# Kernel optimization log

Hardware: AMD Instinct MI355X
Metric: run time of the kernel (lower is better)

Reference implementation:

```python
import jax, jax.numpy as jnp
import numpy as np

D_MODEL, D_QKV, N_HEADS = 1024, 64, 16


def setup_inputs() -> dict:
    key = jax.random.key(0)
    k_x, k_qkv, k_out = jax.random.split(key, 3)
    X = jax.random.normal(k_x, (2, 2048, D_MODEL), dtype=jnp.float32)
    # nn.Linear(d_model, 3*d_qkv*n_heads, bias=False): store as (in, out) for X @ W
    W_qkv = jax.random.normal(k_qkv, (D_MODEL, 3 * D_QKV * N_HEADS), dtype=jnp.float32) * (D_MODEL ** -0.5)
    W_out = jax.random.normal(k_out, (D_QKV * N_HEADS, D_MODEL), dtype=jnp.float32) * ((D_QKV * N_HEADS) ** -0.5)
    return {"X": X, "W_qkv": W_qkv, "W_out": W_out}


def reference(X, W_qkv, W_out):
    b, s, _ = X.shape
    h, d = N_HEADS, D_QKV
    scale = d ** 0.5
    qkv = X @ W_qkv                          # [b, s, 3*h*d]
    # Faithful to torch: view(b, s, h, d, 3).unbind(-1) -> interleaved q/k/v layout
    qkv = qkv.reshape(b, s, h, d, 3)
    q, k, v = qkv[..., 0], qkv[..., 1], qkv[..., 2]   # each [b, s, h, d]
    scores = jnp.einsum("bqhd,bkhd->bhqk", q, k) / scale
    weights = jax.nn.softmax(scores, axis=-1)          # [b, h, s, s]
    attn = jnp.einsum("bhqk,bkhd->bqhd", weights, v)   # [b, s, h, d]
    return attn.reshape(b, s, h * d) @ W_out           # [b, s, d_model]
```

## Files before the change

kernel.cpp:

```cpp
#include <hip/hip_runtime.h>
#include <hip/hip_bf16.h>
#include <math.h>

typedef __bf16 bf16;
typedef __bf16 bf16x2 __attribute__((ext_vector_type(2)));
typedef __bf16 bf16x4 __attribute__((ext_vector_type(4)));
typedef __bf16 bf16x8 __attribute__((ext_vector_type(8)));
typedef float f32x4 __attribute__((ext_vector_type(4)));
typedef float f32x16 __attribute__((ext_vector_type(16)));
typedef int i32x2 __attribute__((ext_vector_type(2)));
typedef int i32x4 __attribute__((ext_vector_type(4)));

#define MFMA16(a, b, c) __builtin_amdgcn_mfma_f32_16x16x32_bf16(a, b, c, 0, 0, 0)
#define MFMA32(a, b, c) __builtin_amdgcn_mfma_f32_32x32x16_bf16(a, b, c, 0, 0, 0)

constexpr int D_MODEL = 1024;
constexpr int N_QKV   = 3072;
constexpr int BATCH   = 2;
constexpr int SEQ     = 2048;
constexpr int NH      = 16;
constexpr int DH      = 64;
constexpr int M_TOT   = BATCH * SEQ;

__device__ __forceinline__ void gl_lds16(const bf16* g, bf16* l) {
    __builtin_amdgcn_global_load_lds(
        (const __attribute__((address_space(1))) void*)g,
        (__attribute__((address_space(3))) void*)l, 16, 0, 0);
}

__device__ __forceinline__ void pl32swap(int& a, int& b) {
    i32x2 r = __builtin_amdgcn_permlane32_swap(a, b, false, false);
    a = r[0];
    b = r[1];
}

__device__ __forceinline__ void transpose_tile(
    const float* __restrict__ in, bf16* __restrict__ out,
    int K, int N, int n0, int k0, bf16 (*T)[72], bool permute)
{
    const int tid = threadIdx.x;
    const int r   = tid >> 2;
    const int c4  = (tid & 3) * 16;

    const float* src = in + (size_t)(k0 + r) * N + n0 + c4;
    f32x4 v0 = *(const f32x4*)(src + 0);
    f32x4 v1 = *(const f32x4*)(src + 4);
    f32x4 v2 = *(const f32x4*)(src + 8);
    f32x4 v3 = *(const f32x4*)(src + 12);
    #pragma unroll
    for (int j = 0; j < 4; j++) {
        T[c4 + j][r]      = (bf16)v0[j];
        T[c4 + 4 + j][r]  = (bf16)v1[j];
        T[c4 + 8 + j][r]  = (bf16)v2[j];
        T[c4 + 12 + j][r] = (bf16)v3[j];
    }
    __syncthreads();
    int rowg = n0 + r;
    if (permute) {
        const int which = rowg % 3;
        const int h     = rowg / 192;
        const int d     = (rowg % 192) / 3;
        rowg = which * 1024 + h * 64 + d;
    }
    bf16* dst = out + (size_t)rowg * K + k0 + c4;
    *(bf16x8*)(dst)     = *(const bf16x8*)&T[r][c4];
    *(bf16x8*)(dst + 8) = *(const bf16x8*)&T[r][c4 + 8];
}

__global__ __launch_bounds__(256) void prepass_kernel(
    const float* __restrict__ X, const float* __restrict__ Wqkv,
    const float* __restrict__ Wout,
    bf16* __restrict__ xb, bf16* __restrict__ wqkv_t, bf16* __restrict__ wout_t)
{
    __shared__ bf16 T[64][72];
    const int b = blockIdx.x;
    if (b < 2048) {
        const size_t i = ((size_t)b * 256 + threadIdx.x) * 8;
        f32x4 a0 = *(const f32x4*)(X + i);
        f32x4 a1 = *(const f32x4*)(X + i + 4);
        bf16x8 w;
        #pragma unroll
        for (int j = 0; j < 4; j++) { w[j] = (bf16)a0[j]; w[j + 4] = (bf16)a1[j]; }
        *(bf16x8*)(xb + i) = w;
    } else if (b < 2048 + 768) {
        const int idx = b - 2048;
        transpose_tile(Wqkv, wqkv_t, D_MODEL, N_QKV,
                       (idx % 48) * 64, (idx / 48) * 64, T, true);
    } else {
        const int idx = b - 2816;
        transpose_tile(Wout, wout_t, D_MODEL, D_MODEL,
                       (idx % 16) * 64, (idx / 16) * 64, T, false);
    }
}

__global__ __launch_bounds__(256) void qkv_gemm_kernel(
    const bf16* __restrict__ Xb, const bf16* __restrict__ Wt,
    bf16* __restrict__ qb, bf16* __restrict__ kb, bf16* __restrict__ vb)
{
    __shared__ __align__(16) bf16 smem[2 * 128 * 64];
    bf16* As = smem;
    bf16* Bs = smem + 128 * 64;

    const int tid  = threadIdx.x;
    const int wave = tid >> 6;
    const int lane = tid & 63;
    const int quad = lane >> 4;
    const int l16  = lane & 15;
    const int sw   = l16 & 7;
    const int m0   = blockIdx.x * 128;
    const int n0   = blockIdx.y * 128;
    const int wm   = (wave & 1) * 64;
    const int wn   = (wave >> 1) * 64;

    const int srow = lane >> 3;
    const int sc_s = ((lane & 7) ^ srow) * 8;
    const int sc_d = (lane & 7) * 8;

    f32x4 acc[4][4];
    #pragma unroll
    for (int a = 0; a < 4; a++)
        #pragma unroll
        for (int b = 0; b < 4; b++) acc[a][b] = {0.f, 0.f, 0.f, 0.f};

    for (int kb0 = 0; kb0 < D_MODEL; kb0 += 64) {
        __syncthreads();
        #pragma unroll
        for (int j = 0; j < 4; j++) {
            const int row = wave * 32 + j * 8 + srow;
            gl_lds16(Xb + (size_t)(m0 + row) * D_MODEL + kb0 + sc_s,
                     As + row * 64 + sc_d);
            gl_lds16(Wt + (size_t)(n0 + row) * D_MODEL + kb0 + sc_s,
                     Bs + row * 64 + sc_d);
        }
        __syncthreads();

        #pragma unroll
        for (int ks = 0; ks < 2; ks++) {
            const int co = ((ks * 4 + quad) ^ sw) * 8;
            bf16x8 af[4], bfr[4];
            #pragma unroll
            for (int mi = 0; mi < 4; mi++)
                af[mi] = *(const bf16x8*)&As[(wm + mi * 16 + l16) * 64 + co];
            #pragma unroll
            for (int ni = 0; ni < 4; ni++)
                bfr[ni] = *(const bf16x8*)&Bs[(wn + ni * 16 + l16) * 64 + co];
            #pragma unroll
            for (int mi = 0; mi < 4; mi++)
                #pragma unroll
                for (int ni = 0; ni < 4; ni++)
                    acc[mi][ni] = MFMA16(af[mi], bfr[ni], acc[mi][ni]);
        }
    }

    const int bb = m0 >> 11;
    if (n0 < 2048) {
        bf16* dst0 = (n0 < 1024) ? qb : kb;
        #pragma unroll
        for (int ni = 0; ni < 4; ni++) {
            const int n = n0 + wn + ni * 16 + l16;
            const int h = (n >> 6) & 15;
            const int d = n & 63;
            #pragma unroll
            for (int mi = 0; mi < 4; mi++) {
                const int s0 = (m0 + wm + mi * 16 + quad * 4) & (SEQ - 1);
                const size_t bh = (size_t)(bb * NH + h);
                #pragma unroll
                for (int i = 0; i < 4; i++)
                    dst0[(bh * SEQ + s0 + i) * DH + d] = (bf16)acc[mi][ni][i];
            }
        }
    } else {
        __syncthreads();
        bf16* T = smem;
        #pragma unroll
        for (int ni = 0; ni < 4; ni++) {
            const int nl = wn + ni * 16 + l16;
            #pragma unroll
            for (int mi = 0; mi < 4; mi++) {
                const int ml = wm + mi * 16 + quad * 4;
                bf16x4 pv;
                #pragma unroll
                for (int i = 0; i < 4; i++) pv[i] = (bf16)acc[mi][ni][i];
                const int c   = ml >> 3;
                const int swz = (c & 8) | ((c ^ nl) & 7);
                *(bf16x4*)&T[nl * 128 + swz * 8 + (ml & 7)] = pv;
            }
        }
        __syncthreads();
        const int hbase  = (n0 - 2048) >> 6;
        const int s_base = m0 & (SEQ - 1);
        #pragma unroll
        for (int it = 0; it < 8; it++) {
            const int nl = (tid >> 4) + it * 16;
            const int mc = tid & 15;
            const int swz = (mc & 8) | ((mc ^ nl) & 7);
            bf16x8 vv = *(const bf16x8*)&T[nl * 128 + swz * 8];
            const int h = hbase + (nl >> 6);
            const int d = nl & 63;
            *(bf16x8*)(vb + ((size_t)(bb * NH + h) * DH + d) * SEQ
                       + s_base + mc * 8) = vv;
        }
    }
}

__global__ __launch_bounds__(256) void attn_kernel(
    const bf16* __restrict__ qb, const bf16* __restrict__ kb,
    const bf16* __restrict__ vb, bf16* __restrict__ ob)
{
    __shared__ __align__(16) bf16 Ks[2][64 * 64];
    __shared__ __align__(16) bf16 Vt[2][64 * 64];

    const int tid  = threadIdx.x;
    const int wave = tid >> 6;
    const int lane = tid & 63;
    const int l32  = lane & 31;
    const int hi   = lane >> 5;
    const int bh   = blockIdx.x;
    const int q0   = blockIdx.y * 128;
    const size_t base = (size_t)bh * SEQ * DH;

    constexpr float QSCALE = 0.125f * 1.44269504f;

    bf16x8 qf[4];
    {
        const size_t qoff = base + (size_t)(q0 + wave * 32 + l32) * DH + hi * 8;
        #pragma unroll
        for (int kc = 0; kc < 4; kc++) {
            qf[kc] = *(const bf16x8*)(qb + qoff + kc * 16);
            #pragma unroll
            for (int j = 0; j < 8; j++)
                qf[kc][j] = (bf16)((float)qf[kc][j] * QSCALE);
        }
    }

    bf16x8 ones;
    #pragma unroll
    for (int j = 0; j < 8; j++) ones[j] = (bf16)1.0f;

    f32x16 o_acc[2];
    f32x16 o_l;
    #pragma unroll
    for (int i = 0; i < 16; i++) {
        o_acc[0][i] = 0.f; o_acc[1][i] = 0.f; o_l[i] = 0.f;
    }

    const int so0 = tid;
    const int so1 = 256 + tid;
    const int sr0 = so0 >> 3, sc0 = ((so0 & 7) ^ (sr0 & 7)) * 8;
    const int sr1 = so1 >> 3, sc1 = ((so1 & 7) ^ (sr1 & 7)) * 8;

    #define STAGE(bufi, kk0)                                                   \
        do {                                                                   \
            gl_lds16(kb + base + (size_t)((kk0) + sr0) * DH + sc0,             \
                     &Ks[bufi][so0 * 8]);                                      \
            gl_lds16(kb + base + (size_t)((kk0) + sr1) * DH + sc1,             \
                     &Ks[bufi][so1 * 8]);                                      \
            gl_lds16(vb + base + (size_t)sr0 * SEQ + (kk0) + sc0,              \
                     &Vt[bufi][so0 * 8]);                                      \
            gl_lds16(vb + base + (size_t)sr1 * SEQ + (kk0) + sc1,              \
                     &Vt[bufi][so1 * 8]);                                      \
        } while (0)

    STAGE(0, 0);
    int buf = 0;

    for (int k0 = 0; k0 < SEQ; k0 += 64) {
        __syncthreads();
        if (k0 + 64 < SEQ) STAGE(buf ^ 1, k0 + 64);

        f32x16 sacc[2];
        #pragma unroll
        for (int i = 0; i < 16; i++) { sacc[0][i] = 0.f; sacc[1][i] = 0.f; }
        #pragma unroll
        for (int kc = 0; kc < 4; kc++) {
            #pragma unroll
            for (int kblk = 0; kblk < 2; kblk++) {
                const int key = kblk * 32 + l32;
                bf16x8 kf = *(const bf16x8*)
                    &Ks[buf][key * 64 + ((2 * kc + hi) ^ (l32 & 7)) * 8];
                sacc[kblk] = MFMA32(kf, qf[kc], sacc[kblk]);
            }
        }

        bf16x8 pa[4];
        #pragma unroll
        for (int kblk = 0; kblk < 2; kblk++) {
            int w[8];
            #pragma unroll
            for (int c = 0; c < 8; c++) {
                bf16x2 t;
                t[0] = (bf16)__builtin_amdgcn_exp2f(sacc[kblk][2 * c]);
                t[1] = (bf16)__builtin_amdgcn_exp2f(sacc[kblk][2 * c + 1]);
                w[c] = __builtin_bit_cast(int, t);
            }
            #pragma unroll
            for (int cc = 0; cc < 2; cc++) {
                pl32swap(w[cc * 4 + 0], w[cc * 4 + 2]);
                pl32swap(w[cc * 4 + 1], w[cc * 4 + 3]);
                i32x4 fi = {w[cc * 4 + 0], w[cc * 4 + 1],
                            w[cc * 4 + 2], w[cc * 4 + 3]};
                pa[kblk * 2 + cc] = __builtin_bit_cast(bf16x8, fi);
            }
        }

        #pragma unroll
        for (int kc = 0; kc < 4; kc++) {
            o_l = MFMA32(pa[kc], ones, o_l);
            #pragma unroll
            for (int nb = 0; nb < 2; nb++) {
                const int d = nb * 32 + l32;
                bf16x8 vf = *(const bf16x8*)
                    &Vt[buf][d * 64 + ((2 * kc + hi) ^ (l32 & 7)) * 8];
                o_acc[nb] = MFMA32(pa[kc], vf, o_acc[nb]);
            }
        }
        buf ^= 1;
    }
    #undef STAGE

    const int b = bh >> 4, h = bh & 15;
    #pragma unroll
    for (int i = 0; i < 16; i++) {
        const int q = q0 + wave * 32 + (i & 3) + 8 * (i >> 2) + 4 * hi;
        const float li = 1.0f / o_l[i];
        #pragma unroll
        for (int nb = 0; nb < 2; nb++)
            ob[((size_t)(b * SEQ + q) * NH + h) * DH + nb * 32 + l32] =
                (bf16)(o_acc[nb][i] * li);
    }
}

__global__ __launch_bounds__(256) void out_gemm_kernel(
    const bf16* __restrict__ A, const bf16* __restrict__ Wt,
    float* __restrict__ out)
{
    __shared__ __align__(16) bf16 As[128 * 64];
    __shared__ __align__(16) bf16 Bs[128 * 64];

    const int tid  = threadIdx.x;
    const int wave = tid >> 6;
    const int lane = tid & 63;
    const int quad = lane >> 4;
    const int l16  = lane & 15;
    const int sw   = l16 & 7;
    const int m0   = blockIdx.x * 128;
    const int n0   = blockIdx.y * 128;
    const int wm   = (wave & 1) * 64;
    const int wn   = (wave >> 1) * 64;

    const int srow = lane >> 3;
    const int sc_s = ((lane & 7) ^ srow) * 8;
    const int sc_d = (lane & 7) * 8;

    f32x4 acc[4][4];
    #pragma unroll
    for (int a = 0; a < 4; a++)
        #pragma unroll
        for (int b = 0; b < 4; b++) acc[a][b] = {0.f, 0.f, 0.f, 0.f};

    for (int kb0 = 0; kb0 < D_MODEL; kb0 += 64) {
        __syncthreads();
        #pragma unroll
        for (int j = 0; j < 4; j++) {
            const int row = wave * 32 + j * 8 + srow;
            gl_lds16(A  + (size_t)(m0 + row) * D_MODEL + kb0 + sc_s,
                     As + row * 64 + sc_d);
            gl_lds16(Wt + (size_t)(n0 + row) * D_MODEL + kb0 + sc_s,
                     Bs + row * 64 + sc_d);
        }
        __syncthreads();

        #pragma unroll
        for (int ks = 0; ks < 2; ks++) {
            const int co = ((ks * 4 + quad) ^ sw) * 8;
            bf16x8 af[4], bfr[4];
            #pragma unroll
            for (int mi = 0; mi < 4; mi++)
                af[mi] = *(const bf16x8*)&As[(wm + mi * 16 + l16) * 64 + co];
            #pragma unroll
            for (int ni = 0; ni < 4; ni++)
                bfr[ni] = *(const bf16x8*)&Bs[(wn + ni * 16 + l16) * 64 + co];
            #pragma unroll
            for (int mi = 0; mi < 4; mi++)
                #pragma unroll
                for (int ni = 0; ni < 4; ni++)
                    acc[mi][ni] = MFMA16(af[mi], bfr[ni], acc[mi][ni]);
        }
    }

    #pragma unroll
    for (int mi = 0; mi < 4; mi++) {
        const int row0 = m0 + wm + mi * 16 + quad * 4;
        #pragma unroll
        for (int ni = 0; ni < 4; ni++) {
            const int n = n0 + wn + ni * 16 + l16;
            #pragma unroll
            for (int i = 0; i < 4; i++)
                out[(size_t)(row0 + i) * D_MODEL + n] = acc[mi][ni][i];
        }
    }
}

extern "C" void kernel_launch(void* const* d_in, const int* in_sizes, int n_in,
                              void* d_out, int out_size, void* d_ws, size_t ws_size,
                              hipStream_t stream)
{
    const float* X    = (const float*)d_in[0];
    const float* Wqkv = (const float*)d_in[1];
    const float* Wout = (const float*)d_in[2];
    float* out        = (float*)d_out;

    const size_t n_elem = (size_t)M_TOT * D_MODEL;
    bf16* qb      = (bf16*)d_ws;
    bf16* kb      = qb + n_elem;
    bf16* vb      = kb + n_elem;
    bf16* attnb   = vb + n_elem;
    bf16* wqkv_t  = attnb + n_elem;
    bf16* wout_t  = wqkv_t + (size_t)N_QKV * D_MODEL;
    bf16* xb      = wout_t + (size_t)D_MODEL * D_MODEL;

    prepass_kernel<<<3072, 256, 0, stream>>>(X, Wqkv, Wout, xb, wqkv_t, wout_t);

    qkv_gemm_kernel<<<dim3(M_TOT / 128, N_QKV / 128), 256, 0, stream>>>(
        xb, wqkv_t, qb, kb, vb);
    attn_kernel<<<dim3(BATCH * NH, SEQ / 128), 256, 0, stream>>>(qb, kb, vb, attnb);
    out_gemm_kernel<<<dim3(M_TOT / 128, D_MODEL / 128), 256, 0, stream>>>(
        attnb, wout_t, out);
}
```

Before: 188.1 us.

## Split attention KV range across two wave groups with LDS merge

The attention kernel now launches 512 threads per block. Two groups of four waves each process half of the key/value sequence for the same 128 queries, and their partial outputs and row sums are merged through shared memory at the end. The softmax denominator is now accumulated with scalar adds plus a cross-half shuffle, replacing the extra MFMA against a ones vector. This doubles the waves available to hide latency and removes MFMA work. In exchange it adds a final LDS reduction, extra barriers, and more register and shared-memory pressure per block.

```diff
diff --git a/kernel.cpp b/kernel.cpp
--- a/kernel.cpp
+++ b/kernel.cpp
@@ -203,27 +203,33 @@
     }
 }
 
-__global__ __launch_bounds__(256) void attn_kernel(
+__global__ __launch_bounds__(512, 4) void attn_kernel(
     const bf16* __restrict__ qb, const bf16* __restrict__ kb,
     const bf16* __restrict__ vb, bf16* __restrict__ ob)
 {
-    __shared__ __align__(16) bf16 Ks[2][64 * 64];
-    __shared__ __align__(16) bf16 Vt[2][64 * 64];
+    __shared__ __align__(16) bf16 smem[32768];
 
     const int tid  = threadIdx.x;
     const int wave = tid >> 6;
+    const int grp  = wave >> 2;
+    const int wq   = wave & 3;
     const int lane = tid & 63;
     const int l32  = lane & 31;
     const int hi   = lane >> 5;
+    const int ltid = tid & 255;
     const int bh   = blockIdx.x;
     const int q0   = blockIdx.y * 128;
-    const size_t base = (size_t)bh * SEQ * DH;
+    const size_t base  = (size_t)bh * SEQ * DH;
+    const int    kbase = grp * (SEQ / 2);
+
+    bf16* const KsB = smem + grp * 2 * 4096;
+    bf16* const VtB = smem + 16384 + grp * 2 * 4096;
 
     constexpr float QSCALE = 0.125f * 1.44269504f;
 
     bf16x8 qf[4];
     {
-        const size_t qoff = base + (size_t)(q0 + wave * 32 + l32) * DH + hi * 8;
+        const size_t qoff = base + (size_t)(q0 + wq * 32 + l32) * DH + hi * 8;
         #pragma unroll
         for (int kc = 0; kc < 4; kc++) {
             qf[kc] = *(const bf16x8*)(qb + qoff + kc * 16);
@@ -233,64 +239,59 @@
         }
     }
 
-    bf16x8 ones;
+    f32x16 o_acc[2];
     #pragma unroll
-    for (int j = 0; j < 8; j++) ones[j] = (bf16)1.0f;
-
-    f32x16 o_acc[2];
-    f32x16 o_l;
-    #pragma unroll
-    for (int i = 0; i < 16; i++) {
-        o_acc[0][i] = 0.f; o_acc[1][i] = 0.f; o_l[i] = 0.f;
-    }
-
-    const int so0 = tid;
-    const int so1 = 256 + tid;
+    for (int i = 0; i < 16; i++) { o_acc[0][i] = 0.f; o_acc[1][i] = 0.f; }
+    float l_acc = 0.f;
+
+    const int so0 = ltid;
+    const int so1 = 256 + ltid;
     const int sr0 = so0 >> 3, sc0 = ((so0 & 7) ^ (sr0 & 7)) * 8;
     const int sr1 = so1 >> 3, sc1 = ((so1 & 7) ^ (sr1 & 7)) * 8;
 
     #define STAGE(bufi, kk0)                                                   \
         do {                                                                   \
-            gl_lds16(kb + base + (size_t)((kk0) + sr0) * DH + sc0,             \
-                     &Ks[bufi][so0 * 8]);                                      \
-            gl_lds16(kb + base + (size_t)((kk0) + sr1) * DH + sc1,             \
-                     &Ks[bufi][so1 * 8]);                                      \
-            gl_lds16(vb + base + (size_t)sr0 * SEQ + (kk0) + sc0,              \
-                     &Vt[bufi][so0 * 8]);                                      \
-            gl_lds16(vb + base + (size_t)sr1 * SEQ + (kk0) + sc1,              \
-                     &Vt[bufi][so1 * 8]);                                      \
+            gl_lds16(kb + base + (size_t)(kbase + (kk0) + sr0) * DH + sc0,     \
+                     KsB + (bufi) * 4096 + so0 * 8);                           \
+            gl_lds16(kb + base + (size_t)(kbase + (kk0) + sr1) * DH + sc1,     \
+                     KsB + (bufi) * 4096 + so1 * 8);                           \
+            gl_lds16(vb + base + (size_t)sr0 * SEQ + kbase + (kk0) + sc0,      \
+                     VtB + (bufi) * 4096 + so0 * 8);                           \
+            gl_lds16(vb + base + (size_t)sr1 * SEQ + kbase + (kk0) + sc1,      \
+                     VtB + (bufi) * 4096 + so1 * 8);                           \
         } while (0)
 
     STAGE(0, 0);
     int buf = 0;
 
-    for (int k0 = 0; k0 < SEQ; k0 += 64) {
-        __syncthreads();
-        if (k0 + 64 < SEQ) STAGE(buf ^ 1, k0 + 64);
-
-        f32x16 sacc[2];
-        #pragma unroll
-        for (int i = 0; i < 16; i++) { sacc[0][i] = 0.f; sacc[1][i] = 0.f; }
-        #pragma unroll
-        for (int kc = 0; kc < 4; kc++) {
-            #pragma unroll
-            for (int kblk = 0; kblk < 2; kblk++) {
-                const int key = kblk * 32 + l32;
+    for (int kt = 0; kt < SEQ / 128; ++kt) {
+        __syncthreads();
+        if (kt + 1 < SEQ / 128) STAGE(buf ^ 1, (kt + 1) * 64);
+
+        const bf16* Kst = KsB + buf * 4096;
+        const bf16* Vtt = VtB + buf * 4096;
+
+        #pragma unroll
+        for (int kblk = 0; kblk < 2; kblk++) {
+            f32x16 sacc;
+            #pragma unroll
+            for (int i = 0; i < 16; i++) sacc[i] = 0.f;
+            #pragma unroll
+            for (int kc = 0; kc < 4; kc++) {
+                const int cko = ((2 * kc + hi) ^ (l32 & 7)) * 8;
                 bf16x8 kf = *(const bf16x8*)
-                    &Ks[buf][key * 64 + ((2 * kc + hi) ^ (l32 & 7)) * 8];
-                sacc[kblk] = MFMA32(kf, qf[kc], sacc[kblk]);
-            }
-        }
-
-        bf16x8 pa[4];
-        #pragma unroll
-        for (int kblk = 0; kblk < 2; kblk++) {
+                    &Kst[(kblk * 32 + l32) * 64 + cko];
+                sacc = MFMA32(kf, qf[kc], sacc);
+            }
+
             int w[8];
             #pragma unroll
             for (int c = 0; c < 8; c++) {
-                bf16x2 t;
-                t[0] = (bf16)__builtin_amdgcn_exp2f(sacc[kblk][2 * c]);
-                t[1] = (bf16)__builtin_amdgcn_exp2f(sacc[kblk][2 * c + 1]);
+                const float e0 = __builtin_amdgcn_exp2f(sacc[2 * c]);
+                const float e1 = __builtin_amdgcn_exp2f(sacc[2 * c + 1]);
+                l_acc += e0;
+                l_acc += e1;
+                bf16x2 t; t[0] = (bf16)e0; t[1] = (bf16)e1;
                 w[c] = __builtin_bit_cast(int, t);
             }
             #pragma unroll
@@ -299,34 +300,68 @@
                 pl32swap(w[cc * 4 + 1], w[cc * 4 + 3]);
                 i32x4 fi = {w[cc * 4 + 0], w[cc * 4 + 1],
                             w[cc * 4 + 2], w[cc * 4 + 3]};
-                pa[kblk * 2 + cc] = __builtin_bit_cast(bf16x8, fi);
-            }
-        }
-
-        #pragma unroll
-        for (int kc = 0; kc < 4; kc++) {
-            o_l = MFMA32(pa[kc], ones, o_l);
-            #pragma unroll
-            for (int nb = 0; nb < 2; nb++) {
-                const int d = nb * 32 + l32;
-                bf16x8 vf = *(const bf16x8*)
-                    &Vt[buf][d * 64 + ((2 * kc + hi) ^ (l32 & 7)) * 8];
-                o_acc[nb] = MFMA32(pa[kc], vf, o_acc[nb]);
+                bf16x8 pa = __builtin_bit_cast(bf16x8, fi);
+
+                const int kc = kblk * 2 + cc;
+                const int cko = ((2 * kc + hi) ^ (l32 & 7)) * 8;
+                #pragma unroll
+                for (int nb = 0; nb < 2; nb++) {
+                    bf16x8 vf = *(const bf16x8*)
+                        &Vtt[(nb * 32 + l32) * 64 + cko];
+                    o_acc[nb] = MFMA32(pa, vf, o_acc[nb]);
+                }
             }
         }
         buf ^= 1;
     }
     #undef STAGE
 
-    const int b = bh >> 4, h = bh & 15;
-    #pragma unroll
-    for (int i = 0; i < 16; i++) {
-        const int q = q0 + wave * 32 + (i & 3) + 8 * (i >> 2) + 4 * hi;
-        const float li = 1.0f / o_l[i];
+    const float l_q = l_acc + __shfl_xor(l_acc, 32);
+
+    float* cO  = (float*)smem;
+    float* cL1 = (float*)smem + 8192;
+    float* cL2 = (float*)smem + 8320;
+
+    __syncthreads();
+    if (grp == 1) {
         #pragma unroll
         for (int nb = 0; nb < 2; nb++)
-            ob[((size_t)(b * SEQ + q) * NH + h) * DH + nb * 32 + l32] =
-                (bf16)(o_acc[nb][i] * li);
+            #pragma unroll
+            for (int c4 = 0; c4 < 4; c4++) {
+                const int j = nb * 4 + c4;
+                f32x4 v = { o_acc[nb][c4 * 4 + 0], o_acc[nb][c4 * 4 + 1],
+                            o_acc[nb][c4 * 4 + 2], o_acc[nb][c4 * 4 + 3] };
+                *(f32x4*)&cO[(wq * 64 + lane) * 32 + ((j ^ (lane & 7)) * 4)] = v;
+            }
+        if (hi == 0) cL1[wq * 32 + l32] = l_q;
+    }
+    __syncthreads();
+    if (grp == 0) {
+        #pragma unroll
+        for (int nb = 0; nb < 2; nb++)
+            #pragma unroll
+            for (int c4 = 0; c4 < 4; c4++) {
+                const int j = nb * 4 + c4;
+                f32x4 v = *(const f32x4*)
+                    &cO[(wq * 64 + lane) * 32 + ((j ^ (lane & 7)) * 4)];
+                #pragma unroll
+                for (int e = 0; e < 4; e++) o_acc[nb][c4 * 4 + e] += v[e];
+            }
+        if (hi == 0) cL2[wq * 32 + l32] = l_q + cL1[wq * 32 + l32];
+    }
+    __syncthreads();
+    if (grp == 0) {
+        const int b = bh >> 4, h = bh & 15;
+        #pragma unroll
+        for (int i = 0; i < 16; i++) {
+            const int qrow = (i & 3) + 8 * (i >> 2) + 4 * hi;
+            const int q = q0 + wq * 32 + qrow;
+            const float li = 1.0f / cL2[wq * 32 + qrow];
+            #pragma unroll
+            for (int nb = 0; nb < 2; nb++)
+                ob[((size_t)(b * SEQ + q) * NH + h) * DH + nb * 32 + l32] =
+                    (bf16)(o_acc[nb][i] * li);
+        }
     }
 }
 
@@ -423,7 +458,7 @@
 
     qkv_gemm_kernel<<<dim3(M_TOT / 128, N_QKV / 128), 256, 0, stream>>>(
         xb, wqkv_t, qb, kb, vb);
-    attn_kernel<<<dim3(BATCH * NH, SEQ / 128), 256, 0, stream>>>(qb, kb, vb, attnb);
+    attn_kernel<<<dim3(BATCH * NH, SEQ / 128), 512, 0, stream>>>(qb, kb, vb, attnb);
     out_gemm_kernel<<<dim3(M_TOT / 128, D_MODEL / 128), 256, 0, stream>>>(
         attnb, wout_t, out);
 }
```

After: 183.9 us. 1.02x faster.
